# Kernel optimization log

Measured on AMD Instinct MI355X. Metric: run time of the kernel, lower is better.

The kernel has to match this reference:

```python
import jax, jax.numpy as jnp
import numpy as np

N_HEADS = 8
TOP_P = 0.5
ALPHA = 0.5
N_VARS = 22

TCP_PAIRS = [('FP1','F7'),('F7','T3'),('T3','T5'),('T5','O1'),('FP2','F8'),('F8','T4'),('T4','T6'),('T6','O2'),('FP1','F3'),('F3','C3'),('C3','P3'),('P3','O1'),('FP2','F4'),('F4','C4'),('C4','P4'),('P4','O2'),('A1','T3'),('T3','C3'),('C3','CZ'),('CZ','C4'),('C4','T4'),('T4','A2')]
E3D = {'FP1':(-0.31,0.95,0.0),'FP2':(0.31,0.95,0.0),'F7':(-0.81,0.59,0.0),'F3':(-0.55,0.67,0.5),'FZ':(0.0,0.71,0.71),'F4':(0.55,0.67,0.5),'F8':(0.81,0.59,0.0),'T3':(-1.0,0.0,0.0),'C3':(-0.57,0.0,0.82),'CZ':(0.0,0.0,1.0),'C4':(0.57,0.0,0.82),'T4':(1.0,0.0,0.0),'T5':(-0.81,-0.59,0.0),'P3':(-0.55,-0.67,0.5),'PZ':(0.0,-0.71,0.71),'P4':(0.55,-0.67,0.5),'T6':(0.81,-0.59,0.0),'O1':(-0.31,-0.95,0.0),'O2':(0.31,-0.95,0.0),'A1':(-1.05,0.0,-0.3),'A2':(1.05,0.0,-0.3)}


def build_region_masks(L, n_vars=N_VARS, spatial_thresh=0.55, temporal_k=3):
    # vectorized numpy equivalent of the torch build_region_masks
    N = L // n_vars
    mid = np.array([(np.array(E3D[a]) + np.array(E3D[b])) / 2.0 for a, b in TCP_PAIRS])
    d = np.linalg.norm(mid[:, None] - mid[None, :], axis=-1)
    ch_adj = (d < spatial_thresh).astype(np.float32)
    np.fill_diagonal(ch_adj, 0.0)
    ch = np.arange(L) // N
    pt = np.arange(L) % N
    S = ch_adj[np.ix_(ch, ch)] * (pt[:, None] == pt[None, :])  # same patch, nearby channel
    dpt = np.abs(pt[:, None] - pt[None, :])
    T = (ch[:, None] == ch[None, :]) * (dpt > 0) * (dpt <= temporal_k) * np.exp(-dpt / float(temporal_k))
    ST = np.clip(1.0 - np.eye(L) - S - T, 0.0, None)
    return np.stack([S, T, ST], axis=1).astype(np.float32)  # [L,3,L]


def layernorm(x, g, b, eps=1e-5):
    m = x.mean(-1, keepdims=True)
    v = ((x - m) ** 2).mean(-1, keepdims=True)
    return (x - m) / jnp.sqrt(v + eps) * g + b


def mask_topk(x, alpha=ALPHA):
    # zero out the alpha-fraction SMALLEST entries per row (torch largest=False)
    L = x.shape[-1]
    k = max(1, int(alpha * L))
    _, idx = jax.lax.top_k(-x, k)              # indices of k smallest
    flat = jnp.ones(x.shape, x.dtype).reshape(-1, L)
    rows = jnp.arange(flat.shape[0])[:, None]
    m = flat.at[rows, idx.reshape(-1, k)].set(0.0)
    return m.reshape(x.shape)


def graph_block(x, masks, ln1_g, ln1_b, w_p1, b_p1, w_p2, b_p2, w_gate,
                w_gcn, b_gcn, ln2_g, ln2_b, w_f1, b_f1, w_f2, b_f2):
    B, L, D = x.shape
    H = N_HEADS
    dh = D // H
    xn = layernorm(x, ln1_g, ln1_b)
    # ---- graph learner: per-head projections, gelu inner product, top-k sparsify
    xh = xn.reshape(B, L, H, dh).transpose(0, 2, 1, 3)          # [B,H,L,dh]
    q = xh @ w_p1 + b_p1
    kk = xh @ w_p2 + b_p2
    adj = jax.nn.gelu(jnp.einsum('bhid,bhjd->bhij', q, kk), approximate=False)
    adj = adj * mask_topk(adj, ALPHA)                            # [B,H,L,L]
    # ---- noisy top-p MoE gating (eval path: no noise)
    af = adj.reshape(B * H, L, L)
    logits = jax.nn.softmax(af @ w_gate, axis=-1)                # [BH,L,3]
    order = jnp.argsort(-logits, axis=-1)                        # descending
    sp = jnp.take_along_axis(logits, order, axis=-1)
    cum = jnp.cumsum(sp, axis=-1)
    m = cum > TOP_P
    thr = jax.nn.one_hot(jnp.argmax(m, axis=-1), 3, dtype=bool)
    m = m & ~thr                                                 # keep first expert crossing top_p
    keep = (~m).astype(jnp.float32)
    inv = jnp.argsort(order, axis=-1)
    gates = jnp.take_along_axis(keep, inv, axis=-1).reshape(B, H, L, 3)
    loss_dyn = -(logits * jnp.log(logits + 1e-10)).sum(1).mean()
    spz = jnp.where(m, 0.0, sp).sum(0)                           # [L,3]
    loss_imp = jnp.var(spz, ddof=1) / (spz.mean() ** 2 + 1e-10)
    loss = loss_imp + 0.1 * loss_dyn
    # ---- mix S/T/ST region masks with gates, add self-loop, mask + softmax
    final_mask = jnp.einsum('bhli,lid->bhld', gates, masks) + jnp.eye(L, dtype=x.dtype)[None, None]
    adj = jax.nn.softmax(adj * final_mask, axis=-1)
    # ---- multi-head graph conv
    xp = (xn @ w_gcn + b_gcn).reshape(B, L, H, dh)
    adjn = adj / jnp.clip(jnp.sum(jnp.abs(adj), axis=-1, keepdims=True), 1e-12)
    out = jnp.einsum('bhij,bjhd->bihd', adjn, xp).reshape(B, L, D)
    # ---- residual + FFN
    x1 = x + out
    xn2 = layernorm(x1, ln2_g, ln2_b)
    ff = jax.nn.gelu(xn2 @ w_f1 + b_f1, approximate=False) @ w_f2 + b_f2
    return x1 + ff, loss


def setup_inputs() -> dict:
    B, L, D, H = 2, 1408, 512, N_HEADS
    dh = D // H
    d_ff = 4 * D
    key = jax.random.key(0)
    ks = jax.random.split(key, 12)
    s = 0.02
    return {
        'x': jax.random.normal(ks[0], (B, L, D), jnp.float32),
        'masks': jnp.asarray(build_region_masks(L)),
        'ln1_g': jnp.ones((D,), jnp.float32),
        'ln1_b': jnp.zeros((D,), jnp.float32),
        'w_p1': s * jax.random.normal(ks[1], (dh, dh), jnp.float32),
        'b_p1': jnp.zeros((dh,), jnp.float32),
        'w_p2': s * jax.random.normal(ks[2], (dh, dh), jnp.float32),
        'b_p2': jnp.zeros((dh,), jnp.float32),
        'w_gate': s * jax.random.normal(ks[3], (L, 3), jnp.float32),
        'w_gcn': s * jax.random.normal(ks[4], (D, D), jnp.float32),
        'b_gcn': jnp.zeros((D,), jnp.float32),
        'ln2_g': jnp.ones((D,), jnp.float32),
        'ln2_b': jnp.zeros((D,), jnp.float32),
        'w_f1': s * jax.random.normal(ks[5], (D, d_ff), jnp.float32),
        'b_f1': jnp.zeros((d_ff,), jnp.float32),
        'w_f2': s * jax.random.normal(ks[6], (d_ff, D), jnp.float32),
        'b_f2': jnp.zeros((D,), jnp.float32),
    }


def reference(x, masks, ln1_g, ln1_b, w_p1, b_p1, w_p2, b_p2, w_gate,
              w_gcn, b_gcn, ln2_g, ln2_b, w_f1, b_f1, w_f2, b_f2):
    return graph_block(x, masks, ln1_g, ln1_b, w_p1, b_p1, w_p2, b_p2, w_gate,
                       w_gcn, b_gcn, ln2_g, ln2_b, w_f1, b_f1, w_f2, b_f2)
```

## Files before the change

kernel.cpp:

```cpp
#include <hip/hip_runtime.h>

#define L_SEQ 1408
#define DMODEL 512
#define NH 8
#define BATCH 2
#define BH 16
#define ROWS 2816
#define DFF 2048
#define KSEL 704

typedef unsigned short u16;
typedef unsigned long long ull;
typedef short s8v __attribute__((ext_vector_type(8)));
typedef float f4v __attribute__((ext_vector_type(4)));

#define SPOPC(b, out) asm("s_bcnt1_i32_b64 %0, %1" : "=s"(out) : "s"(b))
__device__ __forceinline__ ull vcmp_lt_f32(float a, float b){
  ull m;
  asm("v_cmp_lt_f32 %0, %1, %2" : "=s"(m) : "v"(a), "s"(b));
  return m;
}
__device__ __forceinline__ int mbcnt64(ull b){
  return __builtin_amdgcn_mbcnt_hi((unsigned)(b>>32), __builtin_amdgcn_mbcnt_lo((unsigned)b, 0));
}
__device__ __forceinline__ float key2f(unsigned ck){
  unsigned hh = (ck & 0x8000u) ? (ck & 0x7FFFu) : (0xFFFFu & ~ck);
  if ((hh & 0x7FFFu) > 0x7F80u) hh = (hh & 0x8000u) | 0x7F80u;
  return __uint_as_float(hh<<16);
}

__device__ __forceinline__ float gelu_f(float x){
  float u = 1.595769122f*(x + 0.044715f*x*x*x);
  return x * __builtin_amdgcn_rcpf(1.0f + __expf(-u));
}
__device__ __forceinline__ u16 f2bf(float f){
  unsigned u = __float_as_uint(f);
  u += 0x7fffu + ((u>>16)&1u);
  return (u16)(u>>16);
}

__device__ __forceinline__ f4v MFMA(s8v a, s8v b, f4v c){
  return __builtin_amdgcn_mfma_f32_16x16x32_bf16(a, b, c, 0, 0, 0);
}

__device__ __forceinline__ s8v ldfrag(const u16* lds, int row, int kb){
  return *(const s8v*)((const char*)lds + row*128 + ((kb*2) ^ ((row&7)<<4)));
}
__device__ __forceinline__ void stage_tile(const char* g, size_t gstride, u16* lds, int nrows, int t){
  int lane = t&63;
  int nch = nrows*8;
  for (int ci0 = (t>>6)*64; ci0 < nch; ci0 += 256){
    int ci = ci0 + lane;
    int row = ci>>3, j = (ci&7)*16;
    const char* src = g + (size_t)row*gstride + (j ^ ((row&7)<<4));
    u16* dstbase = lds + (size_t)ci0*8;
    __builtin_amdgcn_global_load_lds((const __attribute__((address_space(1))) void*)src,
                                     (__attribute__((address_space(3))) void*)dstbase,
                                     16, 0, 0);
  }
}

__device__ __forceinline__ float block_reduce_sum(float v){
  __shared__ float sred[8];
  int lane = threadIdx.x & 63, w = threadIdx.x >> 6;
  #pragma unroll
  for (int o=32;o>0;o>>=1) v += __shfl_down(v,o,64);
  if (lane==0) sred[w]=v;
  __syncthreads();
  if (w==0){
    float x = (lane < (int)(blockDim.x>>6)) ? sred[lane] : 0.f;
    #pragma unroll
    for (int o=4;o>0;o>>=1) x += __shfl_down(x,o,64);
    if (lane==0) sred[0]=x;
  }
  __syncthreads();
  float r = sred[0];
  __syncthreads();
  return r;
}

__device__ __forceinline__ void ln_body(const float* g, const float* b,
                                        u16* orow, int t, float v0, float v1){
  float s = block_reduce_sum(v0+v1);
  float mean = s * (1.f/512.f);
  float d0 = v0-mean, d1 = v1-mean;
  float ss = block_reduce_sum(d0*d0 + d1*d1);
  float rstd = rsqrtf(ss*(1.f/512.f) + 1e-5f);
  orow[t]     = f2bf(d0*rstd*g[t]     + b[t]);
  orow[t+256] = f2bf(d1*rstd*g[t+256] + b[t+256]);
}

__device__ __forceinline__ void castT_tile(const float* in, u16* outT, int K, int N,
                                           int k0, int n0, int t){
  __shared__ u16 tl[32][33];
  int r = t>>5, c = t&31;
  #pragma unroll
  for (int i=0;i<4;i++){
    int rr = r + i*8;
    tl[rr][c] = f2bf(in[(size_t)(k0+rr)*N + n0 + c]);
  }
  __syncthreads();
  #pragma unroll
  for (int i=0;i<4;i++){
    int rr = r + i*8;
    outT[(size_t)(n0+rr)*K + k0 + c] = tl[c][rr];
  }
}

__global__ __launch_bounds__(256) void prep_kernel(const float* __restrict__ w_gcn, u16* __restrict__ wgcnT,
                                                   const float* __restrict__ w_f1,  u16* __restrict__ wf1T,
                                                   const float* __restrict__ w_f2,  u16* __restrict__ wf2T,
                                                   const float* __restrict__ w_p1,  u16* __restrict__ wp1T,
                                                   const float* __restrict__ w_p2,  u16* __restrict__ wp2T,
                                                   const float* __restrict__ w_gate, float* __restrict__ wgt,
                                                   const float* __restrict__ x,
                                                   const float* __restrict__ g,
                                                   const float* __restrict__ b,
                                                   u16* __restrict__ xn){
  int blk = blockIdx.x, t = threadIdx.x;
  if (blk < 256){
    castT_tile(w_gcn, wgcnT, DMODEL, DMODEL, (blk>>4)*32, (blk&15)*32, t);
  } else if (blk < 1280){
    int lo = blk - 256;
    castT_tile(w_f1, wf1T, DMODEL, DFF, (lo&15)*32, (lo>>4)*32, t);
  } else if (blk < 2304){
    int lo = blk - 1280;
    castT_tile(w_f2, wf2T, DFF, DMODEL, (lo&63)*32, (lo>>6)*32, t);
  } else if (blk < 2308){
    int lo = blk - 2304;
    castT_tile(w_p1, wp1T, 64, 64, (lo>>1)*32, (lo&1)*32, t);
  } else if (blk < 2312){
    int lo = blk - 2308;
    castT_tile(w_p2, wp2T, 64, 64, (lo>>1)*32, (lo&1)*32, t);
  } else if (blk < 2329){
    int idx = (blk-2312)*256 + t;
    if (idx < 3*L_SEQ){
      int j = (idx >= 2*L_SEQ) ? 2 : (idx >= L_SEQ ? 1 : 0);
      int e = idx - j*L_SEQ;
      wgt[idx] = w_gate[e*3 + j];
    }
  } else {
    int row = blk - 2329;
    const float* xr = x + (size_t)row*DMODEL;
    ln_body(g, b, xn + (size_t)row*DMODEL, t, xr[t], xr[t+256]);
  }
}

__global__ __launch_bounds__(256) void ln2_fuse_kernel(const float* __restrict__ x,
                                                       const float* __restrict__ P,
                                                       const float* __restrict__ g,
                                                       const float* __restrict__ b,
                                                       float* __restrict__ x1,
                                                       u16* __restrict__ xn2){
  int row = blockIdx.x, t = threadIdx.x;
  size_t base = (size_t)row*DMODEL;
  const float* P1 = P + (size_t)ROWS*DMODEL;
  float v0 = x[base+t]     + P[base+t]     + P1[base+t];
  float v1 = x[base+t+256] + P[base+t+256] + P1[base+t+256];
  x1[base+t] = v0; x1[base+t+256] = v1;
  ln_body(g, b, xn2 + base, t, v0, v1);
}

__global__ __launch_bounds__(256) void qk_mfma_kernel(const u16* __restrict__ xn,
                                                      const u16* __restrict__ wp1T,
                                                      const u16* __restrict__ wp2T,
                                                      const float* __restrict__ bp1,
                                                      const float* __restrict__ bp2,
                                                      u16* __restrict__ q, u16* __restrict__ k){
  __shared__ u16 As[128*64], W1[64*64], W2[64*64];
  int m0 = blockIdx.x*128;
  int t = threadIdx.x, lane=t&63, w=t>>6;
  stage_tile((const char*)xn + (size_t)m0*128, 128, As, 128, t);
  stage_tile((const char*)wp1T, 128, W1, 64, t);
  stage_tile((const char*)wp2T, 128, W2, 64, t);
  __syncthreads();
  int fr=lane&15, kb=(lane>>4)*8;
  f4v aq[2][4], ak[2][4];
  #pragma unroll
  for (int mi=0;mi<2;mi++)
    #pragma unroll
    for (int n=0;n<4;n++){ aq[mi][n]=(f4v){0.f,0.f,0.f,0.f}; ak[mi][n]=(f4v){0.f,0.f,0.f,0.f}; }
  #pragma unroll
  for (int kk=0;kk<2;kk++){
    s8v a[2], b1[4], b2[4];
    #pragma unroll
    for (int mi=0;mi<2;mi++) a[mi] = ldfrag(As, w*32+mi*16+fr, kk*32+kb);
    #pragma unroll
    for (int n=0;n<4;n++){ b1[n]=ldfrag(W1, n*16+fr, kk*32+kb); b2[n]=ldfrag(W2, n*16+fr, kk*32+kb); }
    #pragma unroll
    for (int mi=0;mi<2;mi++)
      #pragma unroll
      for (int n=0;n<4;n++){
        aq[mi][n] = MFMA(a[mi], b1[n], aq[mi][n]);
        ak[mi][n] = MFMA(a[mi], b2[n], ak[mi][n]);
      }
  }
  #pragma unroll
  for (int mi=0;mi<2;mi++){
    #pragma unroll
    for (int n=0;n<4;n++){
      int j = n*16 + fr;
      float bq = bp1[j], bk = bp2[j];
      #pragma unroll
      for (int r=0;r<4;r++){
        int m = m0 + w*32 + mi*16 + (lane>>4)*4 + r;
        int bl = m>>3, h = m&7;
        int b_ = bl / L_SEQ, l = bl - b_*L_SEQ;
        size_t o = (((size_t)(b_*NH+h))*L_SEQ + l)*64 + j;
        q[o] = f2bf(aq[mi][n][r] + bq);
        k[o] = f2bf(ak[mi][n][r] + bk);
      }
    }
  }
}

__global__ __launch_bounds__(256) void qkt_mfma_kernel(const u16* __restrict__ q,
                                                       const u16* __restrict__ k,
                                                       u16* __restrict__ adj){
  __shared__ u16 sbuf[128*128];
  u16* Qs = sbuf; u16* Ks = sbuf + 128*64; u16* Cs = sbuf;
  int z = blockIdx.z;
  int i0 = blockIdx.x*128, j0 = blockIdx.y*128;
  int t = threadIdx.x;
  const char* Qb = (const char*)(q + (size_t)z*L_SEQ*64) + (size_t)i0*128;
  const char* Kb = (const char*)(k + (size_t)z*L_SEQ*64) + (size_t)j0*128;
  stage_tile(Qb, 128, Qs, 128, t);
  stage_tile(Kb, 128, Ks, 128, t);
  __syncthreads();
  int lane = t&63, w = t>>6, wm = w>>1, wn = w&1;
  int fr = lane&15, kb = (lane>>4)*8;
  f4v acc[4][4];
  #pragma unroll
  for (int m=0;m<4;m++)
    #pragma unroll
    for (int n=0;n<4;n++) acc[m][n]=(f4v){0.f,0.f,0.f,0.f};
  #pragma unroll
  for (int kk=0;kk<2;kk++){
    s8v a[4], bv[4];
    #pragma unroll
    for (int m=0;m<4;m++) a[m] = ldfrag(Qs, wm*64+m*16+fr, kk*32+kb);
    #pragma unroll
    for (int n=0;n<4;n++) bv[n] = ldfrag(Ks, wn*64+n*16+fr, kk*32+kb);
    #pragma unroll
    for (int m=0;m<4;m++)
      #pragma unroll
      for (int n=0;n<4;n++) acc[m][n] = MFMA(a[m], bv[n], acc[m][n]);
  }
  __syncthreads();
  #pragma unroll
  for (int m=0;m<4;m++){
    int row = wm*64 + m*16 + (lane>>4)*4;
    #pragma unroll
    for (int n=0;n<4;n++){
      int col = wn*64 + n*16 + fr;
      #pragma unroll
      for (int r=0;r<4;r++)
        Cs[(row+r)*128 + col] = f2bf(gelu_f(acc[m][n][r]));
    }
  }
  __syncthreads();
  u16* Cb = adj + (size_t)z*L_SEQ*L_SEQ;
  #pragma unroll
  for (int i=0;i<8;i++){
    int idx = i*256 + t;
    int r = idx>>4, cc = (idx&15)*8;
    uint4 v = *(const uint4*)&Cs[r*128 + cc];
    *(uint4*)((char*)Cb + (size_t)(i0+r)*2816 + (j0+cc)*2) = v;
  }
}

template<int OUTBF16,int ACT,int TRANSOUT>
__global__ __launch_bounds__(256) void gemm_mfma_kernel(const u16* __restrict__ A,
                                                        const u16* __restrict__ BT,
                                                        const float* __restrict__ bias,
                                                        void* __restrict__ outp,
                                                        int M, int N, int K){
  __shared__ u16 As[128*64], Bs[128*64];
  int i0 = blockIdx.x*128, j0 = blockIdx.y*128;
  int t = threadIdx.x, lane=t&63, w=t>>6, wm=w>>1, wn=w&1;
  int fr=lane&15, kb=(lane>>4)*8;
  f4v acc[4][4];
  #pragma unroll
  for (int m=0;m<4;m++)
    #pragma unroll
    for (int n=0;n<4;n++) acc[m][n]=(f4v){0.f,0.f,0.f,0.f};
  size_t strA=(size_t)K*2;
  const char* Ab = (const char*)A + (size_t)i0*strA;
  const char* Bb = (const char*)BT + (size_t)j0*strA;
  for (int k0=0;k0<K;k0+=64){
    stage_tile(Ab + (size_t)k0*2, strA, As, 128, t);
    stage_tile(Bb + (size_t)k0*2, strA, Bs, 128, t);
    __syncthreads();
    #pragma unroll
    for (int kk=0;kk<2;kk++){
      s8v a[4], bv[4];
      #pragma unroll
      for (int m=0;m<4;m++) a[m]=ldfrag(As, wm*64+m*16+fr, kk*32+kb);
      #pragma unroll
      for (int n=0;n<4;n++) bv[n]=ldfrag(Bs, wn*64+n*16+fr, kk*32+kb);
      #pragma unroll
      for (int m=0;m<4;m++)
        #pragma unroll
        for (int n=0;n<4;n++) acc[m][n]=MFMA(a[m],bv[n],acc[m][n]);
    }
    __syncthreads();
  }
  #pragma unroll
  for (int m=0;m<4;m++){
    int row = i0 + wm*64+m*16+(lane>>4)*4;
    #pragma unroll
    for (int n=0;n<4;n++){
      int col = j0 + wn*64+n*16+fr;
      float bb = bias[col];
      #pragma unroll
      for (int r=0;r<4;r++){
        float v = acc[m][n][r]+bb;
        if (ACT) v = gelu_f(v);
        if (TRANSOUT) ((u16*)outp)[(size_t)col*M + row + r] = f2bf(v);
        else if (OUTBF16) ((u16*)outp)[(size_t)(row+r)*N+col] = f2bf(v);
        else ((float*)outp)[(size_t)(row+r)*N+col] = v;
      }
    }
  }
}

__global__ __launch_bounds__(256) void gemm_ks_kernel(const u16* __restrict__ A,
                                                      const u16* __restrict__ BT,
                                                      float* __restrict__ P,
                                                      int M, int N, int K, int KS){
  __shared__ u16 As[128*64], Bs[128*64];
  int i0 = blockIdx.x*128, j0 = blockIdx.y*128;
  int kbeg = blockIdx.z*KS;
  int t = threadIdx.x, lane=t&63, w=t>>6, wm=w>>1, wn=w&1;
  int fr=lane&15, kb=(lane>>4)*8;
  f4v acc[4][4];
  #pragma unroll
  for (int m=0;m<4;m++)
    #pragma unroll
    for (int n=0;n<4;n++) acc[m][n]=(f4v){0.f,0.f,0.f,0.f};
  size_t strA=(size_t)K*2;
  const char* Ab = (const char*)A + (size_t)i0*strA;
  const char* Bb = (const char*)BT + (size_t)j0*strA;
  for (int k0=kbeg; k0<kbeg+KS; k0+=64){
    stage_tile(Ab + (size_t)k0*2, strA, As, 128, t);
    stage_tile(Bb + (size_t)k0*2, strA, Bs, 128, t);
    __syncthreads();
    #pragma unroll
    for (int kk=0;kk<2;kk++){
      s8v a[4], bv[4];
      #pragma unroll
      for (int m=0;m<4;m++) a[m]=ldfrag(As, wm*64+m*16+fr, kk*32+kb);
      #pragma unroll
      for (int n=0;n<4;n++) bv[n]=ldfrag(Bs, wn*64+n*16+fr, kk*32+kb);
      #pragma unroll
      for (int m=0;m<4;m++)
        #pragma unroll
        for (int n=0;n<4;n++) acc[m][n]=MFMA(a[m],bv[n],acc[m][n]);
    }
    __syncthreads();
  }
  float* Pz = P + (size_t)blockIdx.z*M*N;
  #pragma unroll
  for (int m=0;m<4;m++){
    int row = i0 + wm*64+m*16+(lane>>4)*4;
    #pragma unroll
    for (int n=0;n<4;n++){
      int col = j0 + wn*64+n*16+fr;
      #pragma unroll
      for (int r=0;r<4;r++) Pz[(size_t)(row+r)*N+col] = acc[m][n][r];
    }
  }
}

__global__ __launch_bounds__(256) void gc_ks_kernel(const u16* __restrict__ adj,
                                                    const u16* __restrict__ xpt,
                                                    float* __restrict__ P){
  __shared__ u16 As[128*64], Bs[64*64];
  int z = blockIdx.z, b = z>>3, h = z&7;
  int i0 = blockIdx.x*128;
  int kbeg = blockIdx.y*704;
  int t = threadIdx.x, lane=t&63, w=t>>6, wm=w>>1, wn=w&1;
  int fr=lane&15, kb=(lane>>4)*8;
  const char* Ab = (const char*)(adj + (size_t)z*L_SEQ*L_SEQ) + (size_t)i0*2816;
  const char* Bb = (const char*)xpt + (size_t)(h*64)*5632 + (size_t)(b*L_SEQ)*2;
  f4v acc[4][2];
  #pragma unroll
  for (int m=0;m<4;m++){ acc[m][0]=(f4v){0.f,0.f,0.f,0.f}; acc[m][1]=(f4v){0.f,0.f,0.f,0.f}; }
  for (int k0=kbeg; k0<kbeg+704; k0+=64){
    stage_tile(Ab + (size_t)k0*2, 2816, As, 128, t);
    stage_tile(Bb + (size_t)k0*2, 5632, Bs, 64, t);
    __syncthreads();
    #pragma unroll
    for (int kk=0;kk<2;kk++){
      s8v a[4], bv[2];
      #pragma unroll
      for (int m=0;m<4;m++) a[m]=ldfrag(As, wm*64+m*16+fr, kk*32+kb);
      #pragma unroll
      for (int n=0;n<2;n++) bv[n]=ldfrag(Bs, wn*32+n*16+fr, kk*32+kb);
      #pragma unroll
      for (int m=0;m<4;m++)
        #pragma unroll
        for (int n=0;n<2;n++) acc[m][n]=MFMA(a[m],bv[n],acc[m][n]);
    }
    __syncthreads();
  }
  float* Pz = P + (size_t)blockIdx.y*ROWS*DMODEL;
  #pragma unroll
  for (int m=0;m<4;m++){
    int rl = i0 + wm*64+m*16+(lane>>4)*4;
    #pragma unroll
    for (int n=0;n<2;n++){
      int col = h*64 + wn*32+n*16+fr;
      #pragma unroll
      for (int r=0;r<4;r++)
        Pz[(size_t)(b*L_SEQ + rl + r)*DMODEL + col] = acc[m][n][r];
    }
  }
}

__global__ __launch_bounds__(256) void row_pipe2_kernel(u16* __restrict__ adj,
                                                        const float* __restrict__ wgt,
                                                        const float* __restrict__ masks,
                                                        float* __restrict__ spz,
                                                        float* __restrict__ entp){
  __shared__ float smask[3*L_SEQ];
  int t = threadIdx.x, lane = t&63, w = t>>6;
  int l = blockIdx.x >> 2;
  int z = (blockIdx.x & 3)*4 + w;
  int rid = z*L_SEQ + l;
  unsigned* rowp = (unsigned*)(adj + (size_t)rid*L_SEQ);

  const char* msrc = (const char*)(masks + (size_t)l*3*L_SEQ);
  for (int ci0 = w*64; ci0 < 1056; ci0 += 256){
    int ci = ci0 + lane;
    if (ci < 1056)
      __builtin_amdgcn_global_load_lds((const __attribute__((address_space(1))) void*)(msrc + (size_t)ci*16),
                                       (__attribute__((address_space(3))) void*)((char*)smask + (size_t)ci0*16),
                                       16, 0, 0);
  }

  float x0[11], x1[11];
  #pragma unroll
  for (int i=0;i<11;i++){
    unsigned r = rowp[i*64 + lane];
    x0[i] = __uint_as_float(r<<16);
    x1[i] = __uint_as_float(r & 0xFFFF0000u);
  }

  unsigned thr_k = 0; int cnt_thr = 0;
  #pragma unroll
  for (int b=15;b>=0;b--){
    unsigned ck = thr_k | (1u<<b);
    float cf = key2f(ck);
    int cnt = 0;
    #pragma unroll
    for (int i=0;i<11;i++){
      ull b0 = vcmp_lt_f32(x0[i], cf);
      ull b1 = vcmp_lt_f32(x1[i], cf);
      int c0, c1; SPOPC(b0, c0); SPOPC(b1, c1);
      cnt += c0 + c1;
    }
    if ((unsigned)cnt < KSEL){ thr_k = ck; cnt_thr = cnt; }
  }
  float thr_f = key2f(thr_k);
  int z_eq = KSEL - cnt_thr;

  int cnt = 0;
  #pragma unroll
  for (int i=0;i<11;i++){
    bool eq0 = (x0[i]==thr_f);
    bool eq1 = (x1[i]==thr_f);
    ull b0 = __ballot(eq0), b1 = __ballot(eq1);
    int p0b = mbcnt64(b0), p1b = mbcnt64(b1);
    int pre0 = p0b + p1b;
    int pre1 = pre0 + (eq0?1:0);
    if (eq0 && cnt+pre0 < z_eq) x0[i]=0.f;
    if (eq1 && cnt+pre1 < z_eq) x1[i]=0.f;
    if (x0[i] < thr_f) x0[i]=0.f;
    if (x1[i] < thr_f) x1[i]=0.f;
    int c0, c1; SPOPC(b0, c0); SPOPC(b1, c1);
    cnt += c0 + c1;
  }

  const float* wg0 = wgt;
  const float* wg1 = wgt + L_SEQ;
  const float* wg2 = wgt + 2*L_SEQ;
  float p0=0.f, p1=0.f, p2=0.f;
  #pragma unroll
  for (int i=0;i<11;i++){
    int e0 = 2*(i*64+lane);
    float2 w0 = *(const float2*)&wg0[e0];
    float2 w1 = *(const float2*)&wg1[e0];
    float2 w2 = *(const float2*)&wg2[e0];
    p0 += x0[i]*w0.x + x1[i]*w0.y;
    p1 += x0[i]*w1.x + x1[i]*w1.y;
    p2 += x0[i]*w2.x + x1[i]*w2.y;
  }
  #pragma unroll
  for (int o=1;o<64;o<<=1){
    p0 += __shfl_xor(p0,o,64);
    p1 += __shfl_xor(p1,o,64);
    p2 += __shfl_xor(p2,o,64);
  }
  float e0s=__expf(p0), e1s=__expf(p1), e2s=__expf(p2);
  float inv = __builtin_amdgcn_rcpf(e0s+e1s+e2s);
  float pr[3]={e0s*inv, e1s*inv, e2s*inv};
  int i0=0; if (pr[1]>pr[i0]) i0=1; if (pr[2]>pr[i0]) i0=2;
  int a_=(i0==0)?1:0, b_=(i0==2)?1:2;
  int i1 = (pr[b_]>pr[a_])?b_:a_;
  bool top2 = !(pr[i0] > 0.5f);
  bool g0=(i0==0)||(top2&&i1==0);
  bool g1=(i0==1)||(top2&&i1==1);
  bool g2=(i0==2)||(top2&&i1==2);
  if (lane==0){
    float ent = pr[0]*__logf(pr[0]+1e-10f)+pr[1]*__logf(pr[1]+1e-10f)+pr[2]*__logf(pr[2]+1e-10f);
    atomicAdd(&entp[rid & 255], ent);
    atomicAdd(&spz[l*3+0], pr[i0]);
    if (top2) atomicAdd(&spz[l*3+1], pr[i1]);
  }

  __syncthreads();
  int offA = g0 ? 0 : (g1 ? L_SEQ : 2*L_SEQ);
  int offB = offA; float sB = 0.f;
  if (g0 && g1){ offB = L_SEQ; sB = 1.f; }
  else if (g0 && g2){ offB = 2*L_SEQ; sB = 1.f; }
  else if (g1 && g2){ offB = 2*L_SEQ; sB = 1.f; }
  int i_self = l>>7, lane_self = (l>>1)&63, slot = l&1;
  float mself = (lane==lane_self) ? 1.f : 0.f;
  float sum=0.f;
  #pragma unroll
  for (int i=0;i<11;i++){
    int e0 = 2*(i*64+lane);
    float2 va = *(const float2*)&smask[offA + e0];
    float2 vb = *(const float2*)&smask[offB + e0];
    float fm0 = va.x + sB*vb.x;
    float fm1 = va.y + sB*vb.y;
    if (i == i_self){
      if (slot==0) fm0 += mself; else fm1 += mself;
    }
    x0[i] = __expf(x0[i]*fm0);
    x1[i] = __expf(x1[i]*fm1);
    sum += x0[i]+x1[i];
  }
  #pragma unroll
  for (int o=1;o<64;o<<=1) sum += __shfl_xor(sum,o,64);
  float invs = __builtin_amdgcn_rcpf(sum);
  #pragma unroll
  for (int i=0;i<11;i++){
    unsigned lo = f2bf(x0[i]*invs), hi = f2bf(x1[i]*invs);
    rowp[i*64+lane] = lo | (hi<<16);
  }
}

__global__ __launch_bounds__(256) void final_kernel(const float* __restrict__ P,
                                                    const float* __restrict__ x1,
                                                    const float* __restrict__ bias,
                                                    const float* __restrict__ spz,
                                                    const float* __restrict__ entp,
                                                    float* __restrict__ out){
  int t = threadIdx.x;
  if (blockIdx.x < 1408){
    int idx = blockIdx.x*256 + t;
    const float4* P0 = (const float4*)P;
    const float4* P1 = (const float4*)(P + (size_t)ROWS*DMODEL);
    const float4* X  = (const float4*)x1;
    const float4* B4 = (const float4*)bias;
    float4 a = P0[idx], b = P1[idx], c = X[idx], d = B4[idx & 127];
    float4 o; o.x=a.x+b.x+c.x+d.x; o.y=a.y+b.y+c.y+d.y; o.z=a.z+b.z+c.z+d.z; o.w=a.w+b.w+c.w+d.w;
    ((float4*)out)[idx] = o;
  } else {
    float sum=0.f;
    for (int i=t;i<4224;i+=256) sum += spz[i];
    sum = block_reduce_sum(sum);
    float mu = sum/4224.f;
    float ss=0.f;
    for (int i=t;i<4224;i+=256){ float d=spz[i]-mu; ss+=d*d; }
    ss = block_reduce_sum(ss);
    float ent = block_reduce_sum(entp[t]);
    if (t==0){
      float var = ss/4223.f;
      float li = var/(mu*mu+1e-10f);
      float ld = -ent/48.f;
      out[(size_t)ROWS*DMODEL] = li + 0.1f*ld;
    }
  }
}

extern "C" void kernel_launch(void* const* d_in, const int* in_sizes, int n_in,
                              void* d_out, int out_size, void* d_ws, size_t ws_size,
                              hipStream_t stream) {
  const float* x     = (const float*)d_in[0];
  const float* masks = (const float*)d_in[1];
  const float* ln1_g = (const float*)d_in[2];
  const float* ln1_b = (const float*)d_in[3];
  const float* w_p1  = (const float*)d_in[4];
  const float* b_p1  = (const float*)d_in[5];
  const float* w_p2  = (const float*)d_in[6];
  const float* b_p2  = (const float*)d_in[7];
  const float* w_gate= (const float*)d_in[8];
  const float* w_gcn = (const float*)d_in[9];
  const float* b_gcn = (const float*)d_in[10];
  const float* ln2_g = (const float*)d_in[11];
  const float* ln2_b = (const float*)d_in[12];
  const float* w_f1  = (const float*)d_in[13];
  const float* b_f1  = (const float*)d_in[14];
  const float* w_f2  = (const float*)d_in[15];
  const float* b_f2  = (const float*)d_in[16];
  float* out = (float*)d_out;

  char* wsb = (char*)d_ws;
  size_t off = 0;
  u16* adj   = (u16*)(wsb+off); off += (size_t)BH*L_SEQ*L_SEQ*2;
  u16* xn    = (u16*)(wsb+off); off += (size_t)ROWS*DMODEL*2;
  u16* q     = (u16*)(wsb+off); off += (size_t)BH*L_SEQ*64*2;
  u16* kk    = (u16*)(wsb+off); off += (size_t)BH*L_SEQ*64*2;
  u16* xpt   = (u16*)(wsb+off); off += (size_t)DMODEL*ROWS*2;
  u16* xn2   = (u16*)(wsb+off); off += (size_t)ROWS*DMODEL*2;
  float* x1  = (float*)(wsb+off); off += (size_t)ROWS*DMODEL*4;
  float* Pk  = (float*)(wsb+off); off += (size_t)2*ROWS*DMODEL*4;
  u16* wgcnT = (u16*)(wsb+off); off += (size_t)DMODEL*DMODEL*2;
  u16* wf1T  = (u16*)(wsb+off); off += (size_t)DFF*DMODEL*2;
  u16* wf2T  = (u16*)(wsb+off); off += (size_t)DMODEL*DFF*2;
  u16* wp1T  = (u16*)(wsb+off); off += (size_t)64*64*2;
  u16* wp2T  = (u16*)(wsb+off); off += (size_t)64*64*2;
  float* wgt = (float*)(wsb+off); off += (size_t)3*L_SEQ*4;
  float* spz = (float*)(wsb+off); off += 4224*4;
  float* entp= (float*)(wsb+off); off += 256*4;
  u16* ffh   = adj;

  hipMemsetAsync(spz, 0, (4224+256)*sizeof(float), stream);

  prep_kernel<<<dim3(2329+ROWS), 256, 0, stream>>>(w_gcn, wgcnT, w_f1, wf1T, w_f2, wf2T,
                                                   w_p1, wp1T, w_p2, wp2T, w_gate, wgt,
                                                   x, ln1_g, ln1_b, xn);
  qk_mfma_kernel<<<dim3(176), 256, 0, stream>>>(xn, wp1T, wp2T, b_p1, b_p2, q, kk);
  qkt_mfma_kernel<<<dim3(11,11,BH), 256, 0, stream>>>(q, kk, adj);
  row_pipe2_kernel<<<dim3(L_SEQ*4), 256, 0, stream>>>(adj, wgt, masks, spz, entp);
  gemm_mfma_kernel<0,0,1><<<dim3(22,4), 256, 0, stream>>>(xn, wgcnT, b_gcn, xpt, ROWS, DMODEL, DMODEL);
  gc_ks_kernel<<<dim3(11,2,BH), 256, 0, stream>>>(adj, xpt, Pk);
  ln2_fuse_kernel<<<ROWS, 256, 0, stream>>>(x, Pk, ln2_g, ln2_b, x1, xn2);
  gemm_mfma_kernel<1,1,0><<<dim3(22,16), 256, 0, stream>>>(xn2, wf1T, b_f1, ffh, ROWS, DFF, DMODEL);
  gemm_ks_kernel<<<dim3(22,4,2), 256, 0, stream>>>(ffh, wf2T, Pk, ROWS, DMODEL, DFF, DFF/2);
  final_kernel<<<dim3(1409), 256, 0, stream>>>(Pk, x1, b_f2, spz, entp, out);
}
```

Measured before the change: 187.7 us.

## Fuse GCN projection GEMM into QK^T launch and use radix-4 threshold search

The x·W_gcn projection GEMM now runs as extra blocks (z=16 slice) of the QK^T kernel, removing a separate launch and letting the two independent workloads share the GPU. The row top-k threshold bisection now resolves two bits per step with three comparisons, halving the number of sequential dependent rounds at the cost of more compares per round. The extra slice wastes 33 of its 121 blocks, which return immediately.

Measured after the change: 198.9 us. 1.06x slower.

```diff
diff --git a/kernel.cpp b/kernel.cpp
--- a/kernel.cpp
+++ b/kernel.cpp
@@ -214,58 +214,107 @@
   }
 }
 
-__global__ __launch_bounds__(256) void qkt_mfma_kernel(const u16* __restrict__ q,
+__global__ __launch_bounds__(256) void qkt_plus_kernel(const u16* __restrict__ q,
                                                        const u16* __restrict__ k,
-                                                       u16* __restrict__ adj){
+                                                       u16* __restrict__ adj,
+                                                       const u16* __restrict__ xn,
+                                                       const u16* __restrict__ wgcnT,
+                                                       const float* __restrict__ b_gcn,
+                                                       u16* __restrict__ xpt){
   __shared__ u16 sbuf[128*128];
-  u16* Qs = sbuf; u16* Ks = sbuf + 128*64; u16* Cs = sbuf;
-  int z = blockIdx.z;
-  int i0 = blockIdx.x*128, j0 = blockIdx.y*128;
-  int t = threadIdx.x;
-  const char* Qb = (const char*)(q + (size_t)z*L_SEQ*64) + (size_t)i0*128;
-  const char* Kb = (const char*)(k + (size_t)z*L_SEQ*64) + (size_t)j0*128;
-  stage_tile(Qb, 128, Qs, 128, t);
-  stage_tile(Kb, 128, Ks, 128, t);
-  __syncthreads();
-  int lane = t&63, w = t>>6, wm = w>>1, wn = w&1;
+  int t = threadIdx.x, lane = t&63, w = t>>6;
   int fr = lane&15, kb = (lane>>4)*8;
-  f4v acc[4][4];
-  #pragma unroll
-  for (int m=0;m<4;m++)
-    #pragma unroll
-    for (int n=0;n<4;n++) acc[m][n]=(f4v){0.f,0.f,0.f,0.f};
-  #pragma unroll
-  for (int kk=0;kk<2;kk++){
-    s8v a[4], bv[4];
-    #pragma unroll
-    for (int m=0;m<4;m++) a[m] = ldfrag(Qs, wm*64+m*16+fr, kk*32+kb);
-    #pragma unroll
-    for (int n=0;n<4;n++) bv[n] = ldfrag(Ks, wn*64+n*16+fr, kk*32+kb);
+  if (blockIdx.z < 16){
+    u16* Qs = sbuf; u16* Ks = sbuf + 128*64; u16* Cs = sbuf;
+    int z = blockIdx.z;
+    int i0 = blockIdx.x*128, j0 = blockIdx.y*128;
+    const char* Qb = (const char*)(q + (size_t)z*L_SEQ*64) + (size_t)i0*128;
+    const char* Kb = (const char*)(k + (size_t)z*L_SEQ*64) + (size_t)j0*128;
+    stage_tile(Qb, 128, Qs, 128, t);
+    stage_tile(Kb, 128, Ks, 128, t);
+    __syncthreads();
+    int wm = w>>1, wn = w&1;
+    f4v acc[4][4];
     #pragma unroll
     for (int m=0;m<4;m++)
       #pragma unroll
-      for (int n=0;n<4;n++) acc[m][n] = MFMA(a[m], bv[n], acc[m][n]);
-  }
-  __syncthreads();
-  #pragma unroll
-  for (int m=0;m<4;m++){
-    int row = wm*64 + m*16 + (lane>>4)*4;
-    #pragma unroll
-    for (int n=0;n<4;n++){
-      int col = wn*64 + n*16 + fr;
-      #pragma unroll
-      for (int r=0;r<4;r++)
-        Cs[(row+r)*128 + col] = f2bf(gelu_f(acc[m][n][r]));
-    }
-  }
-  __syncthreads();
-  u16* Cb = adj + (size_t)z*L_SEQ*L_SEQ;
-  #pragma unroll
-  for (int i=0;i<8;i++){
-    int idx = i*256 + t;
-    int r = idx>>4, cc = (idx&15)*8;
-    uint4 v = *(const uint4*)&Cs[r*128 + cc];
-    *(uint4*)((char*)Cb + (size_t)(i0+r)*2816 + (j0+cc)*2) = v;
+      for (int n=0;n<4;n++) acc[m][n]=(f4v){0.f,0.f,0.f,0.f};
+    #pragma unroll
+    for (int kk=0;kk<2;kk++){
+      s8v a[4], bv[4];
+      #pragma unroll
+      for (int m=0;m<4;m++) a[m] = ldfrag(Qs, wm*64+m*16+fr, kk*32+kb);
+      #pragma unroll
+      for (int n=0;n<4;n++) bv[n] = ldfrag(Ks, wn*64+n*16+fr, kk*32+kb);
+      #pragma unroll
+      for (int m=0;m<4;m++)
+        #pragma unroll
+        for (int n=0;n<4;n++) acc[m][n] = MFMA(a[m], bv[n], acc[m][n]);
+    }
+    __syncthreads();
+    #pragma unroll
+    for (int m=0;m<4;m++){
+      int row = wm*64 + m*16 + (lane>>4)*4;
+      #pragma unroll
+      for (int n=0;n<4;n++){
+        int col = wn*64 + n*16 + fr;
+        #pragma unroll
+        for (int r=0;r<4;r++)
+          Cs[(row+r)*128 + col] = f2bf(gelu_f(acc[m][n][r]));
+      }
+    }
+    __syncthreads();
+    u16* Cb = adj + (size_t)z*L_SEQ*L_SEQ;
+    #pragma unroll
+    for (int i=0;i<8;i++){
+      int idx = i*256 + t;
+      int r = idx>>4, cc = (idx&15)*8;
+      uint4 v = *(const uint4*)&Cs[r*128 + cc];
+      *(uint4*)((char*)Cb + (size_t)(i0+r)*2816 + (j0+cc)*2) = v;
+    }
+  } else {
+    int idx = blockIdx.y*11 + blockIdx.x;
+    if (idx >= 88) return;
+    int i0 = (idx>>2)*128, j0 = (idx&3)*128;
+    u16* As = sbuf; u16* Bs = sbuf + 128*64;
+    int wm = w>>1, wn = w&1;
+    f4v acc[4][4];
+    #pragma unroll
+    for (int m=0;m<4;m++)
+      #pragma unroll
+      for (int n=0;n<4;n++) acc[m][n]=(f4v){0.f,0.f,0.f,0.f};
+    const char* Ab = (const char*)xn + (size_t)i0*1024;
+    const char* Bb = (const char*)wgcnT + (size_t)j0*1024;
+    for (int k0=0;k0<DMODEL;k0+=64){
+      stage_tile(Ab + (size_t)k0*2, 1024, As, 128, t);
+      stage_tile(Bb + (size_t)k0*2, 1024, Bs, 128, t);
+      __syncthreads();
+      #pragma unroll
+      for (int kk=0;kk<2;kk++){
+        s8v a[4], bv[4];
+        #pragma unroll
+        for (int m=0;m<4;m++) a[m]=ldfrag(As, wm*64+m*16+fr, kk*32+kb);
+        #pragma unroll
+        for (int n=0;n<4;n++) bv[n]=ldfrag(Bs, wn*64+n*16+fr, kk*32+kb);
+        #pragma unroll
+        for (int m=0;m<4;m++)
+          #pragma unroll
+          for (int n=0;n<4;n++) acc[m][n]=MFMA(a[m],bv[n],acc[m][n]);
+      }
+      __syncthreads();
+    }
+    #pragma unroll
+    for (int m=0;m<4;m++){
+      int row = i0 + wm*64+m*16+(lane>>4)*4;
+      #pragma unroll
+      for (int n=0;n<4;n++){
+        int col = j0 + wn*64+n*16+fr;
+        float bb = b_gcn[col];
+        #pragma unroll
+        for (int r=0;r<4;r++)
+          xpt[(size_t)col*ROWS + row + r] = f2bf(acc[m][n][r]+bb);
+      }
+    }
   }
 }
 
@@ -449,18 +498,25 @@
 
   unsigned thr_k = 0; int cnt_thr = 0;
   #pragma unroll
-  for (int b=15;b>=0;b--){
-    unsigned ck = thr_k | (1u<<b);
-    float cf = key2f(ck);
-    int cnt = 0;
+  for (int b=14;b>=0;b-=2){
+    unsigned c1k = thr_k | (1u<<b), c2k = thr_k | (2u<<b), c3k = thr_k | (3u<<b);
+    float f1 = key2f(c1k), f2 = key2f(c2k), f3 = key2f(c3k);
+    int n1=0, n2=0, n3=0;
     #pragma unroll
     for (int i=0;i<11;i++){
-      ull b0 = vcmp_lt_f32(x0[i], cf);
-      ull b1 = vcmp_lt_f32(x1[i], cf);
-      int c0, c1; SPOPC(b0, c0); SPOPC(b1, c1);
-      cnt += c0 + c1;
-    }
-    if ((unsigned)cnt < KSEL){ thr_k = ck; cnt_thr = cnt; }
+      ull mA1 = vcmp_lt_f32(x0[i], f1), mB1 = vcmp_lt_f32(x1[i], f1);
+      ull mA2 = vcmp_lt_f32(x0[i], f2), mB2 = vcmp_lt_f32(x1[i], f2);
+      ull mA3 = vcmp_lt_f32(x0[i], f3), mB3 = vcmp_lt_f32(x1[i], f3);
+      int q0,q1,q2,q3,q4,q5;
+      SPOPC(mA1,q0); SPOPC(mB1,q1); SPOPC(mA2,q2); SPOPC(mB2,q3); SPOPC(mA3,q4); SPOPC(mB3,q5);
+      n1 += q0+q1; n2 += q2+q3; n3 += q4+q5;
+    }
+    if ((unsigned)n2 < KSEL){
+      if ((unsigned)n3 < KSEL){ thr_k = c3k; cnt_thr = n3; }
+      else                    { thr_k = c2k; cnt_thr = n2; }
+    } else {
+      if ((unsigned)n1 < KSEL){ thr_k = c1k; cnt_thr = n1; }
+    }
   }
   float thr_f = key2f(thr_k);
   int z_eq = KSEL - cnt_thr;
@@ -634,9 +690,8 @@
                                                    w_p1, wp1T, w_p2, wp2T, w_gate, wgt,
                                                    x, ln1_g, ln1_b, xn);
   qk_mfma_kernel<<<dim3(176), 256, 0, stream>>>(xn, wp1T, wp2T, b_p1, b_p2, q, kk);
-  qkt_mfma_kernel<<<dim3(11,11,BH), 256, 0, stream>>>(q, kk, adj);
+  qkt_plus_kernel<<<dim3(11,11,17), 256, 0, stream>>>(q, kk, adj, xn, wgcnT, b_gcn, xpt);
   row_pipe2_kernel<<<dim3(L_SEQ*4), 256, 0, stream>>>(adj, wgt, masks, spz, entp);
-  gemm_mfma_kernel<0,0,1><<<dim3(22,4), 256, 0, stream>>>(xn, wgcnT, b_gcn, xpt, ROWS, DMODEL, DMODEL);
   gc_ks_kernel<<<dim3(11,2,BH), 256, 0, stream>>>(adj, xpt, Pk);
   ln2_fuse_kernel<<<ROWS, 256, 0, stream>>>(x, Pk, ln2_g, ln2_b, x1, xn2);
   gemm_mfma_kernel<1,1,0><<<dim3(22,16), 256, 0, stream>>>(xn2, wf1T, b_f1, ffh, ROWS, DFF, DMODEL);
```
